# Kernel tuning notes

Hardware: AMD Instinct MI355X
Metric: run time of the kernel (lower is better)

The kernel has to match this reference:

```python
import jax, jax.numpy as jnp
import numpy as np

N = 100000   # nodes
E = 1000000  # edges
IN = 100     # input feature dim
H = 4        # heads
D = 32       # hidden per head (H*D = 128)
C = 47       # classes
EPS = 1e-5
SLOPE = 0.2  # DGL GATv2 leaky_relu negative slope


def setup_inputs() -> dict:
    key = jax.random.key(0)
    ks = jax.random.split(key, 32)
    lin = lambda k, i, o: (jax.random.normal(k, (i, o), jnp.float32) / np.float32(np.sqrt(i)))
    inp = {}
    inp['x'] = jax.random.normal(ks[0], (N, IN), jnp.float32)
    inp['src'] = jax.random.randint(ks[1], (E,), 0, N, jnp.int32)
    inp['dst'] = jnp.sort(jax.random.randint(ks[2], (E,), 0, N, jnp.int32))
    # layer 0: IN -> H*D, Linear residual (IN != H*D)
    inp['Wsrc0'] = lin(ks[3], IN, H * D); inp['bsrc0'] = jnp.zeros(H * D, jnp.float32)
    inp['Wdst0'] = lin(ks[4], IN, H * D); inp['bdst0'] = jnp.zeros(H * D, jnp.float32)
    inp['attn0'] = lin(ks[5], H, D)
    inp['Wres0'] = lin(ks[6], IN, H * D); inp['bres0'] = jnp.zeros(H * D, jnp.float32)
    # layer 1: H*D -> H*D, Identity residual (128 == 128)
    inp['Wsrc1'] = lin(ks[7], H * D, H * D); inp['bsrc1'] = jnp.zeros(H * D, jnp.float32)
    inp['Wdst1'] = lin(ks[8], H * D, H * D); inp['bdst1'] = jnp.zeros(H * D, jnp.float32)
    inp['attn1'] = lin(ks[9], H, D)
    # layer 2: H*D -> H*C, Linear residual (128 != 188)
    inp['Wsrc2'] = lin(ks[10], H * D, H * C); inp['bsrc2'] = jnp.zeros(H * C, jnp.float32)
    inp['Wdst2'] = lin(ks[11], H * D, H * C); inp['bdst2'] = jnp.zeros(H * C, jnp.float32)
    inp['attn2'] = lin(ks[12], H, C)
    inp['Wres2'] = lin(ks[13], H * D, H * C); inp['bres2'] = jnp.zeros(H * C, jnp.float32)
    # BatchNorm1d params (training-mode batch stats)
    inp['g0'] = jnp.ones(H * D, jnp.float32); inp['be0'] = jnp.zeros(H * D, jnp.float32)
    inp['g1'] = jnp.ones(H * D, jnp.float32); inp['be1'] = jnp.zeros(H * D, jnp.float32)
    return inp


def _gatv2(h, src, dst, Ws, bs, Wd, bd, attn, resval):
    """One GATv2Conv on a full block (src feats == dst feats == h)."""
    Hh, Dd = attn.shape
    fs = (h @ Ws + bs).reshape(-1, Hh, Dd)   # [N,H,D] src projection
    fd = (h @ Wd + bd).reshape(-1, Hh, Dd)   # [N,H,D] dst projection
    e = jax.nn.leaky_relu(fs[src] + fd[dst], SLOPE)         # [E,H,D]
    logits = jnp.einsum('ehd,hd->eh', e, attn)              # [E,H]
    m = jax.ops.segment_max(logits, dst, num_segments=N)    # per-dst max
    ex = jnp.exp(logits - m[dst])
    s = jax.ops.segment_sum(ex, dst, num_segments=N)
    alpha = ex / s[dst]                                      # edge softmax
    out = jax.ops.segment_sum(alpha[:, :, None] * fs[src], dst, num_segments=N)
    return out + resval                                      # [N,H,D]


def _bn(x, g, b):
    mu = x.mean(0)
    v = x.var(0)  # biased, as torch BN training mode
    return g * (x - mu) / jnp.sqrt(v + EPS) + b


def reference(x, src, dst,
              Wsrc0, bsrc0, Wdst0, bdst0, attn0, Wres0, bres0,
              Wsrc1, bsrc1, Wdst1, bdst1, attn1,
              Wsrc2, bsrc2, Wdst2, bdst2, attn2, Wres2, bres2,
              g0, be0, g1, be1):
    # layer 0: conv(+relu activation) -> flatten -> BN -> relu (dropout = eval identity)
    res0 = (x @ Wres0 + bres0).reshape(N, H, D)
    h = jax.nn.relu(_gatv2(x, src, dst, Wsrc0, bsrc0, Wdst0, bdst0, attn0, res0))
    h = jax.nn.relu(_bn(h.reshape(N, H * D), g0, be0))
    # layer 1: Identity residual
    res1 = h.reshape(N, H, D)
    h = jax.nn.relu(_gatv2(h, src, dst, Wsrc1, bsrc1, Wdst1, bdst1, attn1, res1))
    h = jax.nn.relu(_bn(h.reshape(N, H * D), g1, be1))
    # layer 2: no activation; mean over heads; log_softmax
    res2 = (h @ Wres2 + bres2).reshape(N, H, C)
    h = _gatv2(h, src, dst, Wsrc2, bsrc2, Wdst2, bdst2, attn2, res2)
    h = h.mean(1)                                # [N,C]
    return jax.nn.log_softmax(h, axis=-1)
```

## Files before the change

### kernel.cpp

```cpp
#include <hip/hip_runtime.h>
#include <hip/hip_bf16.h>

#define Nn 100000
#define Ee 1000000
#define INF_ 100
#define Hh 4
#define Dd 32
#define HD 128
#define Cc 47
#define HC 188
#define HCP 192
#define EPSV 1e-5f
#define SLOPE 0.2f
#define NBLK ((Nn + 255) / 256)

typedef __hip_bfloat16 bf16;
typedef __attribute__((ext_vector_type(8))) short short8;
typedef __attribute__((ext_vector_type(4))) float f32x4;

__device__ __forceinline__ float tof(bf16 v) { return __bfloat162float(v); }
__device__ __forceinline__ float b2f(unsigned short u) {
    return __uint_as_float((unsigned)u << 16);
}
__device__ __forceinline__ float ldb(const bf16* p) {
    return b2f(*(const unsigned short*)p);
}
__device__ __forceinline__ unsigned short f2u(float v) {
    bf16 t = __float2bfloat16(v);
    return *(unsigned short*)&t;
}

template <int C>
__device__ __forceinline__ float dppadd(float v) {
    int m = __builtin_amdgcn_update_dpp(0, __float_as_int(v), C, 0xF, 0xF, false);
    return v + __int_as_float(m);
}
template <int C>
__device__ __forceinline__ float dppmax(float v) {
    int m = __builtin_amdgcn_update_dpp(0, __float_as_int(v), C, 0xF, 0xF, false);
    return fmaxf(v, __int_as_float(m));
}
__device__ __forceinline__ float sum16(float p) {
    p = dppadd<0xB1>(p);
    p = dppadd<0x4E>(p);
    p = dppadd<0x124>(p);
    p = dppadd<0x128>(p);
    return p;
}
__device__ __forceinline__ float max16(float p) {
    p = dppmax<0xB1>(p); p = dppmax<0x4E>(p);
    p = dppmax<0x124>(p); p = dppmax<0x128>(p);
    return p;
}

#define L2E 1.4426950408889634f

__global__ void detect_dtype(const unsigned* __restrict__ x, int* __restrict__ flag) {
    if (blockIdx.x == 0 && threadIdx.x == 0) {
        int good = 0;
        for (int i = 0; i < 256; ++i) {
            unsigned lo = x[i] & 0xFFFFu;
            float v = __uint_as_float(lo << 16);
            float a = fabsf(v);
            if (a > 1e-4f && a < 10.f) good++;
        }
        *flag = (good >= 128) ? 1 : 0;
    }
}

__device__ __forceinline__ float ld_any(const void* p, int i, int isbf) {
    return isbf ? tof(((const bf16*)p)[i]) : ((const float*)p)[i];
}

__global__ void cvt_x(const void* __restrict__ in, bf16* __restrict__ out,
                      const int* __restrict__ flag) {
    int i = blockIdx.x * blockDim.x + threadIdx.x;
    if (i >= Nn * 128) return;
    int row = i >> 7, col = i & 127;
    float v = (col < INF_) ? ld_any(in, row * INF_ + col, *flag) : 0.f;
    out[i] = __float2bfloat16(v);
}

#define NSP 15
struct CvtTab { const void* src[NSP]; int off[NSP + 1]; };

__global__ void cvt_params(CvtTab t, bf16* __restrict__ out, int total,
                           const int* __restrict__ flag) {
    int i = blockIdx.x * blockDim.x + threadIdx.x;
    if (i >= total) return;
    int isbf = *flag;
    int seg = 0;
    while (i >= t.off[seg + 1]) seg++;
    out[i] = __float2bfloat16(ld_any(t.src[seg], i - t.off[seg], isbf));
}

#define WROWS 1280
struct PrepTab { const void* src[8]; int row0[8]; int K[8]; int M[8]; int MP[8]; };

__global__ void prep_all(PrepTab t, bf16* __restrict__ wtb, const int* __restrict__ flag) {
    int i = blockIdx.x * blockDim.x + threadIdx.x;
    if (i >= WROWS * 128) return;
    int row = i >> 7, k = i & 127;
    int isbf = *flag;
    float v = 0.f;
#pragma unroll
    for (int q = 0; q < 8; ++q) {
        if (row >= t.row0[q] && row < t.row0[q] + t.MP[q]) {
            int m = row - t.row0[q];
            if (m < t.M[q] && k < t.K[q])
                v = ld_any(t.src[q], k * t.M[q] + m, isbf);
        }
    }
    wtb[i] = __float2bfloat16(v);
}

__global__ void zero_u32(unsigned* __restrict__ p, int n) {
    int i = blockIdx.x * blockDim.x + threadIdx.x;
    if (i < n) p[i] = 0u;
}

__global__ void build_ptr(const int* __restrict__ dst, int* __restrict__ ptr) {
    int n = blockIdx.x * blockDim.x + threadIdx.x;
    if (n > Nn) return;
    if (n == Nn) { ptr[Nn] = Ee; return; }
    int lo = 0, hi = Ee;
    while (lo < hi) {
        int mid = (lo + hi) >> 1;
        if (dst[mid] < n) lo = mid + 1; else hi = mid;
    }
    ptr[n] = lo;
}

__global__ void src_scale(const int* __restrict__ src, unsigned* __restrict__ w384,
                          unsigned* __restrict__ w256) {
    int i = blockIdx.x * blockDim.x + threadIdx.x;
    if (i >= Ee) return;
    unsigned s = (unsigned)src[i];
    w384[i] = s * 384u;
    w256[i] = s << 8;
}

__global__ void deg_hist_blk(const int* __restrict__ ptr, int* __restrict__ cnt) {
    __shared__ int lh[256];
    int t = threadIdx.x;
    lh[t] = 0;
    __syncthreads();
    int n = blockIdx.x * 256 + t;
    if (n < Nn) {
        int dg = ptr[n + 1] - ptr[n]; if (dg > 255) dg = 255;
        atomicAdd(&lh[dg], 1);
    }
    __syncthreads();
    cnt[t * NBLK + blockIdx.x] = lh[t];
}

__global__ void deg_scan_blk(const int* __restrict__ cnt, int* __restrict__ base) {
    __shared__ int totals[256];
    int t = threadIdx.x;
    int s = 0;
    for (int k = 0; k < NBLK; ++k) s += cnt[t * NBLK + k];
    totals[t] = s;
    __syncthreads();
    int run = 0;
    for (int b = t + 1; b < 256; ++b) run += totals[b];
    for (int k = 0; k < NBLK; ++k) {
        base[t * NBLK + k] = run;
        run += cnt[t * NBLK + k];
    }
}

__global__ void deg_scatter_blk(const int* __restrict__ ptr, const int* __restrict__ base,
                                int* __restrict__ perm) {
    __shared__ int lh[256];
    int t = threadIdx.x;
    lh[t] = 0;
    __syncthreads();
    int n = blockIdx.x * 256 + t;
    if (n < Nn) {
        int dg = ptr[n + 1] - ptr[n]; if (dg > 255) dg = 255;
        int loc = atomicAdd(&lh[dg], 1);
        perm[base[dg * NBLK + blockIdx.x] + loc] = n;
    }
}

template <int MP, int NOUT, int CS, bool ABN, bool PAD47, int OSTR>
__global__ __launch_bounds__(256, 4) void gemm_big(
    const bf16* __restrict__ A, const bf16* __restrict__ Wt,
    const bf16* __restrict__ b0, const bf16* __restrict__ b1,
    const bf16* __restrict__ b2,
    bf16* __restrict__ o0, bf16* __restrict__ o1, bf16* __restrict__ o2,
    int MR, const float* __restrict__ bnp) {
    __shared__ __align__(16) bf16 Al[64 * 136];
    const int row0 = blockIdx.x * 64;
    const int tid = threadIdx.x;
#pragma unroll
    for (int j = 0; j < 4; ++j) {
        int idx = tid + j * 256;
        int r = idx >> 4, kk = (idx & 15) * 8;
        int4 val = {0, 0, 0, 0};
        if (row0 + r < Nn) {
            val = *(const int4*)&A[(size_t)(row0 + r) * 128 + kk];
            if (ABN) {
                short8 av = *(short8*)&val;
                bf16 tmp[8];
#pragma unroll
                for (int u = 0; u < 8; ++u) {
                    float v = b2f((unsigned short)av[u]);
                    v = fmaxf(fmaf(v, bnp[kk + u], bnp[128 + kk + u]), 0.f);
                    tmp[u] = __float2bfloat16(v);
                }
                val = *(int4*)tmp;
            }
        }
        *(int4*)&Al[r * 136 + kk] = val;
    }
    __syncthreads();
    const int wave = tid >> 6, lane = tid & 63;
    const int n16 = lane & 15, quad = lane >> 4;
    const int colbase = blockIdx.y * (64 * CS) + wave * (16 * CS);
    f32x4 acc[4][CS];
#pragma unroll
    for (int rt = 0; rt < 4; ++rt)
#pragma unroll
        for (int c = 0; c < CS; ++c) acc[rt][c] = (f32x4){0.f, 0.f, 0.f, 0.f};
    const bf16* wb[CS];
#pragma unroll
    for (int c = 0; c < CS; ++c)
        wb[c] = Wt + (size_t)(colbase + c * 16 + n16) * 128 + quad * 8;
    const bf16* ap = Al + n16 * 136 + quad * 8;
#pragma unroll
    for (int ks = 0; ks < 4; ++ks) {
        short8 bf[CS];
#pragma unroll
        for (int c = 0; c < CS; ++c) bf[c] = *(const short8*)(wb[c] + ks * 32);
#pragma unroll
        for (int rt = 0; rt < 4; ++rt) {
            short8 af = *(const short8*)(ap + rt * 16 * 136 + ks * 32);
#pragma unroll
            for (int c = 0; c < CS; ++c)
                acc[rt][c] = __builtin_amdgcn_mfma_f32_16x16x32_bf16(af, bf[c], acc[rt][c], 0, 0, 0);
        }
    }
#pragma unroll
    for (int c = 0; c < CS; ++c) {
        int col = colbase + c * 16 + n16;
        int oi = col / MP, lc = col - oi * MP;
        if (oi >= NOUT || lc >= MR) continue;
        const bf16* bp = (oi == 0) ? b0 : (oi == 1) ? b1 : b2;
        bf16* o = (oi == 0) ? o0 : (oi == 1) ? o1 : o2;
        float bb = tof(bp[lc]);
        int st = PAD47 ? (lc + lc / 47) : lc;
#pragma unroll
        for (int rt = 0; rt < 4; ++rt) {
#pragma unroll
            for (int i = 0; i < 4; ++i) {
                int row = row0 + rt * 16 + quad * 4 + i;
                if (row < Nn)
                    o[(size_t)row * OSTR + st] = __float2bfloat16(acc[rt][c][i] + bb);
            }
        }
    }
}

template <bool RESBN>
__global__ __launch_bounds__(256) void gat_fused_128(
    const bf16* __restrict__ fs, const bf16* __restrict__ fd,
    const unsigned* __restrict__ srcW, const int* __restrict__ ptr,
    const int* __restrict__ perm,
    const bf16* __restrict__ attn, const bf16* __restrict__ resb,
    const float* __restrict__ bnp, bf16* __restrict__ hout) {
    const int wave = threadIdx.x >> 6, lane = threadIdx.x & 63;
    const int di = blockIdx.x * 4 + wave;
    if (di >= Nn) return;
    const int d = perm[di];
    const int c0 = lane * 2;
    const unsigned c0b = (unsigned)c0 * 2u;
    ushort2 aq = *(const ushort2*)&attn[c0];
    float a0 = b2f(aq.x) * L2E, a1 = b2f(aq.y) * L2E;
    float A0 = 0.6f * a0, B0 = 0.4f * a0;
    float A1 = 0.6f * a1, B1 = 0.4f * a1;
    ushort2 dq = *(const ushort2*)&fd[(size_t)d * HD + c0];
    float fd0 = b2f(dq.x), fd1 = b2f(dq.y);
    const char* fsb = (const char*)fs;
    float l = 0.f, O0 = 0.f, O1 = 0.f;
    int e = ptr[d];
    const int e1 = ptr[d + 1];
    for (; e + 3 < e1; e += 4) {
        unsigned vA = srcW[e] + c0b, vB = srcW[e + 1] + c0b;
        unsigned vC = srcW[e + 2] + c0b, vD = srcW[e + 3] + c0b;
        ushort2 qA = *(const ushort2*)(fsb + vA);
        ushort2 qB = *(const ushort2*)(fsb + vB);
        ushort2 qC = *(const ushort2*)(fsb + vC);
        ushort2 qD = *(const ushort2*)(fsb + vD);
        float fA0 = b2f(qA.x), fA1 = b2f(qA.y);
        float fB0 = b2f(qB.x), fB1 = b2f(qB.y);
        float fC0 = b2f(qC.x), fC1 = b2f(qC.y);
        float fD0 = b2f(qD.x), fD1 = b2f(qD.y);
        float xA0 = fA0 + fd0, xA1 = fA1 + fd1;
        float xB0 = fB0 + fd0, xB1 = fB1 + fd1;
        float xC0 = fC0 + fd0, xC1 = fC1 + fd1;
        float xD0 = fD0 + fd0, xD1 = fD1 + fd1;
        float pA = fmaf(xA0, A0, fmaf(fabsf(xA0), B0, fmaf(xA1, A1, fabsf(xA1) * B1)));
        float pB = fmaf(xB0, A0, fmaf(fabsf(xB0), B0, fmaf(xB1, A1, fabsf(xB1) * B1)));
        float pC = fmaf(xC0, A0, fmaf(fabsf(xC0), B0, fmaf(xC1, A1, fabsf(xC1) * B1)));
        float pD = fmaf(xD0, A0, fmaf(fabsf(xD0), B0, fmaf(xD1, A1, fabsf(xD1) * B1)));
        pA = sum16(pA); pB = sum16(pB); pC = sum16(pC); pD = sum16(pD);
        float eA = __builtin_amdgcn_exp2f(pA), eB = __builtin_amdgcn_exp2f(pB);
        float eC = __builtin_amdgcn_exp2f(pC), eD = __builtin_amdgcn_exp2f(pD);
        l += (eA + eB) + (eC + eD);
        O0 = fmaf(eA, fA0, O0); O0 = fmaf(eB, fB0, O0);
        O0 = fmaf(eC, fC0, O0); O0 = fmaf(eD, fD0, O0);
        O1 = fmaf(eA, fA1, O1); O1 = fmaf(eB, fB1, O1);
        O1 = fmaf(eC, fC1, O1); O1 = fmaf(eD, fD1, O1);
    }
    for (; e < e1; ++e) {
        unsigned v = srcW[e] + c0b;
        ushort2 fq = *(const ushort2*)(fsb + v);
        float f0 = b2f(fq.x), f1 = b2f(fq.y);
        float x0 = f0 + fd0, x1 = f1 + fd1;
        float p = fmaf(x0, A0, fmaf(fabsf(x0), B0, fmaf(x1, A1, fabsf(x1) * B1)));
        p = sum16(p);
        float pe = __builtin_amdgcn_exp2f(p);
        l += pe;
        O0 = fmaf(pe, f0, O0);
        O1 = fmaf(pe, f1, O1);
    }
    float inv = l > 0.f ? 1.f / l : 0.f;
    ushort2 rq = *(const ushort2*)&resb[(size_t)d * HD + c0];
    float r0 = b2f(rq.x), r1 = b2f(rq.y);
    if (RESBN) {
        r0 = fmaxf(fmaf(r0, bnp[c0], bnp[HD + c0]), 0.f);
        r1 = fmaxf(fmaf(r1, bnp[c0 + 1], bnp[HD + c0 + 1]), 0.f);
    }
    float v0 = fmaxf(fmaf(O0, inv, r0), 0.f);
    float v1 = fmaxf(fmaf(O1, inv, r1), 0.f);
    ushort2 ov; ov.x = f2u(v0); ov.y = f2u(v1);
    *(ushort2*)&hout[(size_t)d * HD + c0] = ov;
}

__global__ __launch_bounds__(256) void gat_fused_188(
    const bf16* __restrict__ fs, const bf16* __restrict__ fd,
    const unsigned* __restrict__ srcW, const int* __restrict__ ptr,
    const int* __restrict__ perm,
    const bf16* __restrict__ attn, const bf16* __restrict__ rs,
    void* __restrict__ out, const int* __restrict__ flag) {
    const int wave = threadIdx.x >> 6, lane = threadIdx.x & 63;
    const int di = blockIdx.x * 4 + wave;
    if (di >= Nn) return;
    const int d = perm[di];
    const int h = lane >> 4, j = lane & 15;
    const int c0 = h * 48 + j;
    const unsigned c0b = (unsigned)c0 * 2u;
    const int ca = h * Cc + j;
    const bool has2 = (j < 15);
    float a0 = ldb(&attn[ca]) * L2E;
    float a1 = ldb(&attn[ca + 16]) * L2E;
    float a2 = has2 ? ldb(&attn[ca + 32]) * L2E : 0.f;
    float A0 = 0.6f * a0, B0 = 0.4f * a0;
    float A1 = 0.6f * a1, B1 = 0.4f * a1;
    float A2 = 0.6f * a2, B2 = 0.4f * a2;
    const bf16* fdr = fd + (size_t)d * HCP;
    float fd0 = ldb(&fdr[c0]);
    float fd1 = ldb(&fdr[c0 + 16]);
    float fd2 = ldb(&fdr[c0 + 32]);
    const char* fsb = (const char*)fs;
    float l = 0.f, O0 = 0.f, O1 = 0.f, O2 = 0.f;
    int e = ptr[d];
    const int e1 = ptr[d + 1];
    for (; e + 3 < e1; e += 4) {
        unsigned vA = srcW[e] + c0b, vB = srcW[e + 1] + c0b;
        unsigned vC = srcW[e + 2] + c0b, vD = srcW[e + 3] + c0b;
        float fA0 = b2f(*(const unsigned short*)(fsb + vA));
        float fA1 = b2f(*(const unsigned short*)(fsb + vA + 32));
        float fA2 = b2f(*(const unsigned short*)(fsb + vA + 64));
        float fB0 = b2f(*(const unsigned short*)(fsb + vB));
        float fB1 = b2f(*(const unsigned short*)(fsb + vB + 32));
        float fB2 = b2f(*(const unsigned short*)(fsb + vB + 64));
        float fC0 = b2f(*(const unsigned short*)(fsb + vC));
        float fC1 = b2f(*(const unsigned short*)(fsb + vC + 32));
        float fC2 = b2f(*(const unsigned short*)(fsb + vC + 64));
        float fD0 = b2f(*(const unsigned short*)(fsb + vD));
        float fD1 = b2f(*(const unsigned short*)(fsb + vD + 32));
        float fD2 = b2f(*(const unsigned short*)(fsb + vD + 64));
        float xA0 = fA0 + fd0, xA1 = fA1 + fd1, xA2 = fA2 + fd2;
        float xB0 = fB0 + fd0, xB1 = fB1 + fd1, xB2 = fB2 + fd2;
        float xC0 = fC0 + fd0, xC1 = fC1 + fd1, xC2 = fC2 + fd2;
        float xD0 = fD0 + fd0, xD1 = fD1 + fd1, xD2 = fD2 + fd2;
        float pA = fmaf(xA0, A0, fmaf(fabsf(xA0), B0, fmaf(xA1, A1, fmaf(fabsf(xA1), B1,
                   fmaf(xA2, A2, fabsf(xA2) * B2)))));
        float pB = fmaf(xB0, A0, fmaf(fabsf(xB0), B0, fmaf(xB1, A1, fmaf(fabsf(xB1), B1,
                   fmaf(xB2, A2, fabsf(xB2) * B2)))));
        float pC = fmaf(xC0, A0, fmaf(fabsf(xC0), B0, fmaf(xC1, A1, fmaf(fabsf(xC1), B1,
                   fmaf(xC2, A2, fabsf(xC2) * B2)))));
        float pD = fmaf(xD0, A0, fmaf(fabsf(xD0), B0, fmaf(xD1, A1, fmaf(fabsf(xD1), B1,
                   fmaf(xD2, A2, fabsf(xD2) * B2)))));
        pA = sum16(pA); pB = sum16(pB); pC = sum16(pC); pD = sum16(pD);
        float eA = __builtin_amdgcn_exp2f(pA), eB = __builtin_amdgcn_exp2f(pB);
        float eC = __builtin_amdgcn_exp2f(pC), eD = __builtin_amdgcn_exp2f(pD);
        l += (eA + eB) + (eC + eD);
        O0 = fmaf(eA, fA0, O0); O0 = fmaf(eB, fB0, O0);
        O0 = fmaf(eC, fC0, O0); O0 = fmaf(eD, fD0, O0);
        O1 = fmaf(eA, fA1, O1); O1 = fmaf(eB, fB1, O1);
        O1 = fmaf(eC, fC1, O1); O1 = fmaf(eD, fD1, O1);
        O2 = fmaf(eA, fA2, O2); O2 = fmaf(eB, fB2, O2);
        O2 = fmaf(eC, fC2, O2); O2 = fmaf(eD, fD2, O2);
    }
    for (; e < e1; ++e) {
        unsigned v = srcW[e] + c0b;
        float f0 = b2f(*(const unsigned short*)(fsb + v));
        float f1 = b2f(*(const unsigned short*)(fsb + v + 32));
        float f2 = b2f(*(const unsigned short*)(fsb + v + 64));
        float x0 = f0 + fd0, x1 = f1 + fd1, x2 = f2 + fd2;
        float p = fmaf(x0, A0, fmaf(fabsf(x0), B0, fmaf(x1, A1, fmaf(fabsf(x1), B1,
                  fmaf(x2, A2, fabsf(x2) * B2)))));
        p = sum16(p);
        float pe = __builtin_amdgcn_exp2f(p);
        l += pe;
        O0 = fmaf(pe, f0, O0);
        O1 = fmaf(pe, f1, O1);
        O2 = fmaf(pe, f2, O2);
    }
    float inv = l > 0.f ? 1.f / l : 0.f;
    const bf16* rr = rs + (size_t)d * HCP;
    float v0 = fmaf(O0, inv, ldb(&rr[c0]));
    float v1 = fmaf(O1, inv, ldb(&rr[c0 + 16]));
    float v2 = has2 ? fmaf(O2, inv, ldb(&rr[c0 + 32])) : 0.f;
    v0 += __shfl_xor(v0, 16); v0 += __shfl_xor(v0, 32); v0 *= 0.25f;
    v1 += __shfl_xor(v1, 16); v1 += __shfl_xor(v1, 32); v1 *= 0.25f;
    v2 += __shfl_xor(v2, 16); v2 += __shfl_xor(v2, 32); v2 *= 0.25f;
    float mx = fmaxf(v0, v1);
    if (has2) mx = fmaxf(mx, v2);
    mx = max16(mx);
    float sm = __expf(v0 - mx) + __expf(v1 - mx) + (has2 ? __expf(v2 - mx) : 0.f);
    sm = sum16(sm);
    if (h == 0) {
        float ls = mx + logf(sm);
        if (*flag) {
            bf16* o = (bf16*)out + (size_t)d * Cc;
            o[j] = __float2bfloat16(v0 - ls);
            o[j + 16] = __float2bfloat16(v1 - ls);
            if (has2) o[j + 32] = __float2bfloat16(v2 - ls);
        } else {
            float* o = (float*)out + (size_t)d * Cc;
            o[j] = v0 - ls;
            o[j + 16] = v1 - ls;
            if (has2) o[j + 32] = v2 - ls;
        }
    }
}

__global__ void col_stats(const bf16* __restrict__ in, float* __restrict__ sums) {
    int c = threadIdx.x;
    int r0 = blockIdx.x * 256;
    int r1 = r0 + 256; if (r1 > Nn) r1 = Nn;
    float s = 0.f, s2 = 0.f;
    for (int r = r0; r < r1; ++r) {
        float v = ldb(&in[(size_t)r * HD + c]);
        s += v; s2 += v * v;
    }
    atomicAdd(&sums[c], s);
    atomicAdd(&sums[HD + c], s2);
}

__global__ void bn_finalize(const float* __restrict__ sums, const bf16* __restrict__ g,
                            const bf16* __restrict__ be, float* __restrict__ ss) {
    int c = threadIdx.x;
    float mu = sums[c] * (1.f / Nn);
    float var = sums[HD + c] * (1.f / Nn) - mu * mu;
    float sc = tof(g[c]) * rsqrtf(var + EPSV);
    ss[c] = sc;
    ss[HD + c] = tof(be[c]) - mu * sc;
}

extern "C" void kernel_launch(void* const* d_in, const int* in_sizes, int n_in,
                              void* d_out, int out_size, void* d_ws, size_t ws_size,
                              hipStream_t stream) {
    (void)in_sizes; (void)n_in; (void)out_size; (void)ws_size;
    const void* x = d_in[0];
    const int* src = (const int*)d_in[1];
    const int* dst = (const int*)d_in[2];

    char* ws = (char*)d_ws;
    size_t off = 0;
    auto alloc = [&](size_t bytes) {
        void* p = ws + off;
        off += (bytes + 255) & ~(size_t)255;
        return p;
    };
    bf16* xb = (bf16*)alloc((size_t)Nn * 128 * 2);
    bf16* rb = (bf16*)alloc((size_t)Nn * HD * 2);
    bf16* rs = xb;
    bf16* fs = (bf16*)alloc((size_t)Nn * HCP * 2);
    bf16* fd = (bf16*)alloc((size_t)Nn * HCP * 2);
    bf16* hbA = (bf16*)alloc((size_t)Nn * HD * 2);
    bf16* hbB = (bf16*)alloc((size_t)Nn * HD * 2);
    int* ptr = (int*)alloc((Nn + 1) * 4);
    bf16* wtb = (bf16*)alloc((size_t)WROWS * 128 * 2);
    float* bns = (float*)alloc(2 * HD * 4);
    float* bnss0 = (float*)alloc(2 * HD * 4);
    float* bnss1 = (float*)alloc(2 * HD * 4);
    bf16* pb = (bf16*)alloc(4096 * 2);
    int* flag = (int*)alloc(256);
    unsigned* w384 = (unsigned*)alloc((size_t)Ee * 4);
    unsigned* w256 = (unsigned*)alloc((size_t)Ee * 4);
    int* cnt = (int*)alloc((size_t)256 * NBLK * 4);
    int* cbase = (int*)alloc((size_t)256 * NBLK * 4);
    int* perm = (int*)alloc((size_t)Nn * 4);

    static const int spIdx[NSP] = {4, 6, 7, 9, 11, 13, 14, 16, 18, 19, 21, 22, 23, 24, 25};
    static const int spSz[NSP]  = {HD, HD, HD, HD, HD, HD, HD, HC, HC, HC, HC, HD, HD, HD, HD};
    CvtTab tab;
    int tot = 0;
    for (int i = 0; i < NSP; ++i) { tab.src[i] = d_in[spIdx[i]]; tab.off[i] = tot; tot += spSz[i]; }
    tab.off[NSP] = tot;
    const bf16 *bsrc0 = pb + tab.off[0], *bdst0 = pb + tab.off[1], *attn0 = pb + tab.off[2],
               *bres0 = pb + tab.off[3], *bsrc1 = pb + tab.off[4], *bdst1 = pb + tab.off[5],
               *attn1 = pb + tab.off[6], *bsrc2 = pb + tab.off[7], *bdst2 = pb + tab.off[8],
               *attn2 = pb + tab.off[9], *bres2 = pb + tab.off[10],
               *g0 = pb + tab.off[11], *be0 = pb + tab.off[12],
               *g1 = pb + tab.off[13], *be1 = pb + tab.off[14];

    PrepTab pt;
    static const int wIdx[8] = {3, 5, 8, 10, 12, 15, 17, 20};
    static const int wK[8]   = {INF_, INF_, INF_, HD, HD, HD, HD, HD};
    static const int wM[8]   = {HD, HD, HD, HD, HD, HC, HC, HC};
    static const int wMP[8]  = {128, 128, 128, 128, 128, 192, 192, 192};
    static const int wR0[8]  = {0, 128, 256, 384, 512, 640, 832, 1024};
    for (int i = 0; i < 8; ++i) {
        pt.src[i] = d_in[wIdx[i]]; pt.row0[i] = wR0[i];
        pt.K[i] = wK[i]; pt.M[i] = wM[i]; pt.MP[i] = wMP[i];
    }

    detect_dtype<<<1, 64, 0, stream>>>((const unsigned*)x, flag);
    cvt_x<<<(Nn * 128 + 255) / 256, 256, 0, stream>>>(x, xb, flag);
    cvt_params<<<(tot + 255) / 256, 256, 0, stream>>>(tab, pb, tot, flag);
    prep_all<<<(WROWS * 128 + 255) / 256, 256, 0, stream>>>(pt, wtb, flag);
    build_ptr<<<(Nn + 256) / 256, 256, 0, stream>>>(dst, ptr);
    src_scale<<<(Ee + 255) / 256, 256, 0, stream>>>(src, w384, w256);
    deg_hist_blk<<<NBLK, 256, 0, stream>>>(ptr, cnt);
    deg_scan_blk<<<1, 256, 0, stream>>>(cnt, cbase);
    deg_scatter_blk<<<NBLK, 256, 0, stream>>>(ptr, cbase, perm);

    const int fusedGrid = (Nn + 3) / 4;
    const int statsGrid = (Nn + 255) / 256;
    const int rowBlk = (Nn + 63) / 64;

    gemm_big<128, 3, 3, false, false, HD><<<dim3(rowBlk, 2), 256, 0, stream>>>(
        xb, wtb, bsrc0, bdst0, bres0, fs, fd, rb, HD, nullptr);
    gat_fused_128<false><<<fusedGrid, 256, 0, stream>>>(fs, fd, w256, ptr, perm,
                                                        attn0, rb, nullptr, hbA);
    zero_u32<<<1, 256, 0, stream>>>((unsigned*)bns, 2 * HD);
    col_stats<<<statsGrid, 128, 0, stream>>>(hbA, bns);
    bn_finalize<<<1, HD, 0, stream>>>(bns, g0, be0, bnss0);

    gemm_big<128, 2, 2, true, false, HD><<<dim3(rowBlk, 2), 256, 0, stream>>>(
        hbA, wtb + (size_t)384 * 128, bsrc1, bdst1, nullptr, fs, fd, nullptr, HD, bnss0);
    gat_fused_128<true><<<fusedGrid, 256, 0, stream>>>(fs, fd, w256, ptr, perm,
                                                       attn1, hbA, bnss0, hbB);
    zero_u32<<<1, 256, 0, stream>>>((unsigned*)bns, 2 * HD);
    col_stats<<<statsGrid, 128, 0, stream>>>(hbB, bns);
    bn_finalize<<<1, HD, 0, stream>>>(bns, g1, be1, bnss1);

    gemm_big<192, 3, 3, true, true, HCP><<<dim3(rowBlk, 3), 256, 0, stream>>>(
        hbB, wtb + (size_t)640 * 128, bsrc2, bdst2, bres2, fs, fd, rs, HC, bnss1);
    gat_fused_188<<<fusedGrid, 256, 0, stream>>>(fs, fd, w384, ptr, perm, attn2, rs,
                                                 d_out, flag);
}
```

Baseline: 696.6 us.

## Pack layer-2 head features per lane and drop BN-stat atomics

The layer-2 GEMM now writes src, dst and residual features in a per-lane interleaved layout with a 256-element row stride. Each lane of the 188-wide attention kernel can then fetch its three channels with a single 8-byte load, replacing three scattered 2-byte loads per edge. The source-offset and CSR-pointer kernels are merged into one launch, and the degree-histogram tables are transposed. BatchNorm statistics now go to per-block partials reduced in a finalize kernel, which removes the atomics and the zeroing launch. The wider stride relies on the intermediate buffers being laid out contiguously, because the dst features extend past the original fs/fd allocation.

```diff
diff --git a/kernel.cpp b/kernel.cpp
--- a/kernel.cpp
+++ b/kernel.cpp
@@ -10,6 +10,7 @@
 #define Cc 47
 #define HC 188
 #define HCP 192
+#define PSTR 256
 #define EPSV 1e-5f
 #define SLOPE 0.2f
 #define NBLK ((Nn + 255) / 256)
@@ -21,6 +22,12 @@
 __device__ __forceinline__ float tof(bf16 v) { return __bfloat162float(v); }
 __device__ __forceinline__ float b2f(unsigned short u) {
     return __uint_as_float((unsigned)u << 16);
+}
+__device__ __forceinline__ float b2flo(unsigned u) {
+    return __uint_as_float(u << 16);
+}
+__device__ __forceinline__ float b2fhi(unsigned u) {
+    return __uint_as_float(u & 0xFFFF0000u);
 }
 __device__ __forceinline__ float ldb(const bf16* p) {
     return b2f(*(const unsigned short*)p);
@@ -114,30 +121,24 @@
     wtb[i] = __float2bfloat16(v);
 }
 
-__global__ void zero_u32(unsigned* __restrict__ p, int n) {
+__global__ void src_scale_ptr(const int* __restrict__ src, const int* __restrict__ dst,
+                              unsigned* __restrict__ w512, unsigned* __restrict__ w256,
+                              int* __restrict__ ptr) {
     int i = blockIdx.x * blockDim.x + threadIdx.x;
-    if (i < n) p[i] = 0u;
-}
-
-__global__ void build_ptr(const int* __restrict__ dst, int* __restrict__ ptr) {
-    int n = blockIdx.x * blockDim.x + threadIdx.x;
-    if (n > Nn) return;
-    if (n == Nn) { ptr[Nn] = Ee; return; }
-    int lo = 0, hi = Ee;
-    while (lo < hi) {
-        int mid = (lo + hi) >> 1;
-        if (dst[mid] < n) lo = mid + 1; else hi = mid;
-    }
-    ptr[n] = lo;
-}
-
-__global__ void src_scale(const int* __restrict__ src, unsigned* __restrict__ w384,
-                          unsigned* __restrict__ w256) {
-    int i = blockIdx.x * blockDim.x + threadIdx.x;
-    if (i >= Ee) return;
-    unsigned s = (unsigned)src[i];
-    w384[i] = s * 384u;
-    w256[i] = s << 8;
+    if (i < Ee) {
+        unsigned s = (unsigned)src[i];
+        w512[i] = s << 9;
+        w256[i] = s << 8;
+    }
+    if (i <= Nn) {
+        if (i == Nn) { ptr[Nn] = Ee; return; }
+        int lo = 0, hi = Ee;
+        while (lo < hi) {
+            int mid = (lo + hi) >> 1;
+            if (dst[mid] < i) lo = mid + 1; else hi = mid;
+        }
+        ptr[i] = lo;
+    }
 }
 
 __global__ void deg_hist_blk(const int* __restrict__ ptr, int* __restrict__ cnt) {
@@ -151,21 +152,21 @@
         atomicAdd(&lh[dg], 1);
     }
     __syncthreads();
-    cnt[t * NBLK + blockIdx.x] = lh[t];
+    cnt[blockIdx.x * 256 + t] = lh[t];
 }
 
 __global__ void deg_scan_blk(const int* __restrict__ cnt, int* __restrict__ base) {
     __shared__ int totals[256];
     int t = threadIdx.x;
     int s = 0;
-    for (int k = 0; k < NBLK; ++k) s += cnt[t * NBLK + k];
+    for (int k = 0; k < NBLK; ++k) s += cnt[k * 256 + t];
     totals[t] = s;
     __syncthreads();
     int run = 0;
     for (int b = t + 1; b < 256; ++b) run += totals[b];
     for (int k = 0; k < NBLK; ++k) {
-        base[t * NBLK + k] = run;
-        run += cnt[t * NBLK + k];
+        base[k * 256 + t] = run;
+        run += cnt[k * 256 + t];
     }
 }
 
@@ -179,11 +180,11 @@
     if (n < Nn) {
         int dg = ptr[n + 1] - ptr[n]; if (dg > 255) dg = 255;
         int loc = atomicAdd(&lh[dg], 1);
-        perm[base[dg * NBLK + blockIdx.x] + loc] = n;
-    }
-}
-
-template <int MP, int NOUT, int CS, bool ABN, bool PAD47, int OSTR>
+        perm[base[blockIdx.x * 256 + dg] + loc] = n;
+    }
+}
+
+template <int MP, int NOUT, int CS, bool ABN, bool PACK, int OSTR>
 __global__ __launch_bounds__(256, 4) void gemm_big(
     const bf16* __restrict__ A, const bf16* __restrict__ Wt,
     const bf16* __restrict__ b0, const bf16* __restrict__ b1,
@@ -249,7 +250,13 @@
         const bf16* bp = (oi == 0) ? b0 : (oi == 1) ? b1 : b2;
         bf16* o = (oi == 0) ? o0 : (oi == 1) ? o1 : o2;
         float bb = tof(bp[lc]);
-        int st = PAD47 ? (lc + lc / 47) : lc;
+        int st;
+        if (PACK) {
+            int hh = lc / 47, cc = lc - hh * 47;
+            st = ((hh * 16 + (cc & 15)) << 2) + (cc >> 4);
+        } else {
+            st = lc;
+        }
 #pragma unroll
         for (int rt = 0; rt < 4; ++rt) {
 #pragma unroll
@@ -349,8 +356,7 @@
     if (di >= Nn) return;
     const int d = perm[di];
     const int h = lane >> 4, j = lane & 15;
-    const int c0 = h * 48 + j;
-    const unsigned c0b = (unsigned)c0 * 2u;
+    const unsigned c0b = (unsigned)lane * 8u;
     const int ca = h * Cc + j;
     const bool has2 = (j < 15);
     float a0 = ldb(&attn[ca]) * L2E;
@@ -359,10 +365,11 @@
     float A0 = 0.6f * a0, B0 = 0.4f * a0;
     float A1 = 0.6f * a1, B1 = 0.4f * a1;
     float A2 = 0.6f * a2, B2 = 0.4f * a2;
-    const bf16* fdr = fd + (size_t)d * HCP;
-    float fd0 = ldb(&fdr[c0]);
-    float fd1 = ldb(&fdr[c0 + 16]);
-    float fd2 = ldb(&fdr[c0 + 32]);
+    const char* fdb = (const char*)fd;
+    uint2 dq = *(const uint2*)(fdb + (size_t)d * (PSTR * 2) + c0b);
+    float fd0 = b2flo(dq.x);
+    float fd1 = b2fhi(dq.x);
+    float fd2 = b2flo(dq.y);
     const char* fsb = (const char*)fs;
     float l = 0.f, O0 = 0.f, O1 = 0.f, O2 = 0.f;
     int e = ptr[d];
@@ -370,18 +377,14 @@
     for (; e + 3 < e1; e += 4) {
         unsigned vA = srcW[e] + c0b, vB = srcW[e + 1] + c0b;
         unsigned vC = srcW[e + 2] + c0b, vD = srcW[e + 3] + c0b;
-        float fA0 = b2f(*(const unsigned short*)(fsb + vA));
-        float fA1 = b2f(*(const unsigned short*)(fsb + vA + 32));
-        float fA2 = b2f(*(const unsigned short*)(fsb + vA + 64));
-        float fB0 = b2f(*(const unsigned short*)(fsb + vB));
-        float fB1 = b2f(*(const unsigned short*)(fsb + vB + 32));
-        float fB2 = b2f(*(const unsigned short*)(fsb + vB + 64));
-        float fC0 = b2f(*(const unsigned short*)(fsb + vC));
-        float fC1 = b2f(*(const unsigned short*)(fsb + vC + 32));
-        float fC2 = b2f(*(const unsigned short*)(fsb + vC + 64));
-        float fD0 = b2f(*(const unsigned short*)(fsb + vD));
-        float fD1 = b2f(*(const unsigned short*)(fsb + vD + 32));
-        float fD2 = b2f(*(const unsigned short*)(fsb + vD + 64));
+        uint2 qA = *(const uint2*)(fsb + vA);
+        uint2 qB = *(const uint2*)(fsb + vB);
+        uint2 qC = *(const uint2*)(fsb + vC);
+        uint2 qD = *(const uint2*)(fsb + vD);
+        float fA0 = b2flo(qA.x), fA1 = b2fhi(qA.x), fA2 = b2flo(qA.y);
+        float fB0 = b2flo(qB.x), fB1 = b2fhi(qB.x), fB2 = b2flo(qB.y);
+        float fC0 = b2flo(qC.x), fC1 = b2fhi(qC.x), fC2 = b2flo(qC.y);
+        float fD0 = b2flo(qD.x), fD1 = b2fhi(qD.x), fD2 = b2flo(qD.y);
         float xA0 = fA0 + fd0, xA1 = fA1 + fd1, xA2 = fA2 + fd2;
         float xB0 = fB0 + fd0, xB1 = fB1 + fd1, xB2 = fB2 + fd2;
         float xC0 = fC0 + fd0, xC1 = fC1 + fd1, xC2 = fC2 + fd2;
@@ -407,9 +410,8 @@
     }
     for (; e < e1; ++e) {
         unsigned v = srcW[e] + c0b;
-        float f0 = b2f(*(const unsigned short*)(fsb + v));
-        float f1 = b2f(*(const unsigned short*)(fsb + v + 32));
-        float f2 = b2f(*(const unsigned short*)(fsb + v + 64));
+        uint2 q = *(const uint2*)(fsb + v);
+        float f0 = b2flo(q.x), f1 = b2fhi(q.x), f2 = b2flo(q.y);
         float x0 = f0 + fd0, x1 = f1 + fd1, x2 = f2 + fd2;
         float p = fmaf(x0, A0, fmaf(fabsf(x0), B0, fmaf(x1, A1, fmaf(fabsf(x1), B1,
                   fmaf(x2, A2, fabsf(x2) * B2)))));
@@ -421,10 +423,11 @@
         O2 = fmaf(pe, f2, O2);
     }
     float inv = l > 0.f ? 1.f / l : 0.f;
-    const bf16* rr = rs + (size_t)d * HCP;
-    float v0 = fmaf(O0, inv, ldb(&rr[c0]));
-    float v1 = fmaf(O1, inv, ldb(&rr[c0 + 16]));
-    float v2 = has2 ? fmaf(O2, inv, ldb(&rr[c0 + 32])) : 0.f;
+    const char* rb_ = (const char*)rs;
+    uint2 rq = *(const uint2*)(rb_ + (size_t)d * (PSTR * 2) + c0b);
+    float v0 = fmaf(O0, inv, b2flo(rq.x));
+    float v1 = fmaf(O1, inv, b2fhi(rq.x));
+    float v2 = has2 ? fmaf(O2, inv, b2flo(rq.y)) : 0.f;
     v0 += __shfl_xor(v0, 16); v0 += __shfl_xor(v0, 32); v0 *= 0.25f;
     v1 += __shfl_xor(v1, 16); v1 += __shfl_xor(v1, 32); v1 *= 0.25f;
     v2 += __shfl_xor(v2, 16); v2 += __shfl_xor(v2, 32); v2 *= 0.25f;
@@ -449,7 +452,7 @@
     }
 }
 
-__global__ void col_stats(const bf16* __restrict__ in, float* __restrict__ sums) {
+__global__ void col_stats2(const bf16* __restrict__ in, float* __restrict__ part) {
     int c = threadIdx.x;
     int r0 = blockIdx.x * 256;
     int r1 = r0 + 256; if (r1 > Nn) r1 = Nn;
@@ -458,18 +461,26 @@
         float v = ldb(&in[(size_t)r * HD + c]);
         s += v; s2 += v * v;
     }
-    atomicAdd(&sums[c], s);
-    atomicAdd(&sums[HD + c], s2);
-}
-
-__global__ void bn_finalize(const float* __restrict__ sums, const bf16* __restrict__ g,
-                            const bf16* __restrict__ be, float* __restrict__ ss) {
-    int c = threadIdx.x;
-    float mu = sums[c] * (1.f / Nn);
-    float var = sums[HD + c] * (1.f / Nn) - mu * mu;
-    float sc = tof(g[c]) * rsqrtf(var + EPSV);
-    ss[c] = sc;
-    ss[HD + c] = tof(be[c]) - mu * sc;
+    part[blockIdx.x * 256 + c] = s;
+    part[blockIdx.x * 256 + 128 + c] = s2;
+}
+
+__global__ void bn_finalize2(const float* __restrict__ part, const bf16* __restrict__ g,
+                             const bf16* __restrict__ be, float* __restrict__ ss, int nb) {
+    __shared__ float sh[256];
+    int t = threadIdx.x;
+    int c = t & 127, w = t >> 7;
+    float s = 0.f;
+    for (int k = 0; k < nb; ++k) s += part[k * 256 + w * 128 + c];
+    sh[t] = s;
+    __syncthreads();
+    if (t < 128) {
+        float mu = sh[t] * (1.f / Nn);
+        float var = sh[128 + t] * (1.f / Nn) - mu * mu;
+        float sc = tof(g[t]) * rsqrtf(var + EPSV);
+        ss[t] = sc;
+        ss[HD + t] = tof(be[t]) - mu * sc;
+    }
 }
 
 extern "C" void kernel_launch(void* const* d_in, const int* in_sizes, int n_in,
@@ -494,14 +505,16 @@
     bf16* fd = (bf16*)alloc((size_t)Nn * HCP * 2);
     bf16* hbA = (bf16*)alloc((size_t)Nn * HD * 2);
     bf16* hbB = (bf16*)alloc((size_t)Nn * HD * 2);
+    bf16* fs2 = fs;
+    bf16* fd2 = fs + (size_t)Nn * PSTR;
     int* ptr = (int*)alloc((Nn + 1) * 4);
     bf16* wtb = (bf16*)alloc((size_t)WROWS * 128 * 2);
-    float* bns = (float*)alloc(2 * HD * 4);
+    float* part = (float*)alloc((size_t)NBLK * 256 * 4);
     float* bnss0 = (float*)alloc(2 * HD * 4);
     float* bnss1 = (float*)alloc(2 * HD * 4);
     bf16* pb = (bf16*)alloc(4096 * 2);
     int* flag = (int*)alloc(256);
-    unsigned* w384 = (unsigned*)alloc((size_t)Ee * 4);
+    unsigned* w512 = (unsigned*)alloc((size_t)Ee * 4);
     unsigned* w256 = (unsigned*)alloc((size_t)Ee * 4);
     int* cnt = (int*)alloc((size_t)256 * NBLK * 4);
     int* cbase = (int*)alloc((size_t)256 * NBLK * 4);
@@ -535,34 +548,31 @@
     cvt_x<<<(Nn * 128 + 255) / 256, 256, 0, stream>>>(x, xb, flag);
     cvt_params<<<(tot + 255) / 256, 256, 0, stream>>>(tab, pb, tot, flag);
     prep_all<<<(WROWS * 128 + 255) / 256, 256, 0, stream>>>(pt, wtb, flag);
-    build_ptr<<<(Nn + 256) / 256, 256, 0, stream>>>(dst, ptr);
-    src_scale<<<(Ee + 255) / 256, 256, 0, stream>>>(src, w384, w256);
+    src_scale_ptr<<<(Ee + 255) / 256, 256, 0, stream>>>(src, dst, w512, w256, ptr);
     deg_hist_blk<<<NBLK, 256, 0, stream>>>(ptr, cnt);
     deg_scan_blk<<<1, 256, 0, stream>>>(cnt, cbase);
     deg_scatter_blk<<<NBLK, 256, 0, stream>>>(ptr, cbase, perm);
 
     const int fusedGrid = (Nn + 3) / 4;
-    const int statsGrid = (Nn + 255) / 256;
+    const int statsGrid = NBLK;
     const int rowBlk = (Nn + 63) / 64;
 
     gemm_big<128, 3, 3, false, false, HD><<<dim3(rowBlk, 2), 256, 0, stream>>>(
         xb, wtb, bsrc0, bdst0, bres0, fs, fd, rb, HD, nullptr);
     gat_fused_128<false><<<fusedGrid, 256, 0, stream>>>(fs, fd, w256, ptr, perm,
                                                         attn0, rb, nullptr, hbA);
-    zero_u32<<<1, 256, 0, stream>>>((unsigned*)bns, 2 * HD);
-    col_stats<<<statsGrid, 128, 0, stream>>>(hbA, bns);
-    bn_finalize<<<1, HD, 0, stream>>>(bns, g0, be0, bnss0);
+    col_stats2<<<statsGrid, 128, 0, stream>>>(hbA, part);
+    bn_finalize2<<<1, 256, 0, stream>>>(part, g0, be0, bnss0, statsGrid);
 
     gemm_big<128, 2, 2, true, false, HD><<<dim3(rowBlk, 2), 256, 0, stream>>>(
         hbA, wtb + (size_t)384 * 128, bsrc1, bdst1, nullptr, fs, fd, nullptr, HD, bnss0);
     gat_fused_128<true><<<fusedGrid, 256, 0, stream>>>(fs, fd, w256, ptr, perm,
                                                        attn1, hbA, bnss0, hbB);
-    zero_u32<<<1, 256, 0, stream>>>((unsigned*)bns, 2 * HD);
-    col_stats<<<statsGrid, 128, 0, stream>>>(hbB, bns);
-    bn_finalize<<<1, HD, 0, stream>>>(bns, g1, be1, bnss1);
-
-    gemm_big<192, 3, 3, true, true, HCP><<<dim3(rowBlk, 3), 256, 0, stream>>>(
-        hbB, wtb + (size_t)640 * 128, bsrc2, bdst2, bres2, fs, fd, rs, HC, bnss1);
-    gat_fused_188<<<fusedGrid, 256, 0, stream>>>(fs, fd, w384, ptr, perm, attn2, rs,
+    col_stats2<<<statsGrid, 128, 0, stream>>>(hbB, part);
+    bn_finalize2<<<1, 256, 0, stream>>>(part, g1, be1, bnss1, statsGrid);
+
+    gemm_big<192, 3, 3, true, true, PSTR><<<dim3(rowBlk, 3), 256, 0, stream>>>(
+        hbB, wtb + (size_t)640 * 128, bsrc2, bdst2, bres2, fs2, fd2, rs, HC, bnss1);
+    gat_fused_188<<<fusedGrid, 256, 0, stream>>>(fs2, fd2, w512, ptr, perm, attn2, rs,
                                                  d_out, flag);
 }
```

After: 881.9 us. 1.27x slower.
